# Kernel optimization log

Measured on AMD Instinct MI355X. Metric: run time of the kernel, lower is better.

The kernel has to match this reference:

```python
import jax, jax.numpy as jnp
import numpy as np

S, L, T, E, H = 512, 5, 20, 768, 64


def setup_inputs() -> dict:
    key = jax.random.key(0)
    ks = jax.random.split(key, 32)

    def p(k, shape, scale=0.05):
        return jax.random.normal(k, shape, dtype=jnp.float32) * scale

    return {
        "text_input": jax.random.normal(ks[0], (S, L, T, E), dtype=jnp.float32),
        "time_inputs": jax.random.uniform(ks[1], (S, L, T), dtype=jnp.float32),
        # TimeLSTM per-stock params (gate order f, i, o, c_tmp)
        "Wall": p(ks[2], (S, H, 4 * H)), "bWall": p(ks[3], (S, 4 * H)),
        "Uall": p(ks[4], (S, E, 4 * H)), "bUall": p(ks[5], (S, 4 * H)),
        "Wd": p(ks[6], (S, H, H)), "bWd": p(ks[7], (S, H)),
        # shared text/day Attention per stock
        "W1": p(ks[8], (S, H, H)), "b1": p(ks[9], (S, H)),
        "W2": p(ks[10], (S, H, H)), "b2": p(ks[11], (S, H)),
        "V": p(ks[12], (S, H, 1)), "bV": p(ks[13], (S, 1)),
        # day nn.LSTM per stock (gate order i, f, g, o)
        "Wih": p(ks[14], (S, H, 4 * H)), "Whh": p(ks[15], (S, H, 4 * H)),
        "bih": p(ks[16], (S, 4 * H)), "bhh": p(ks[17], (S, 4 * H)),
        # shared output head
        "lin_w": p(ks[18], (H, 1)), "lin_b": p(ks[19], (1,)),
        "no_stocks": S,
    }


def _forward(text_input, time_inputs, Wall, bWall, Uall, bUall, Wd, bWd,
             W1, b1, W2, b2, V, bV, Wih, Whh, bih, bhh, lin_w, lin_b, no_stocks):
    def per_stock(x, ts, Wall, bWall, Uall, bUall, Wd, bWd,
                  W1, b1, W2, b2, V, bV, Wih, Whh, bih, bhh):
        # x: [L, T, E], ts: [L, T] -- lookback days are an inner batch for the TimeLSTM
        u = jnp.einsum('lte,eg->ltg', x, Uall) + bUall  # [L, T, 4H]

        def step(carry, inp):
            h, c = carry                 # [L, H]
            u_t, ts_t = inp              # [L, 4H], [L]
            c_s1 = jnp.tanh(c @ Wd + bWd)
            c_adj = (c - c_s1) + c_s1 * ts_t[:, None]
            gates = h @ Wall + bWall + u_t
            f, i, o, c_tmp = jnp.split(gates, 4, axis=1)
            f = jax.nn.sigmoid(f)
            i = jax.nn.sigmoid(i)
            o = jax.nn.sigmoid(o)
            c_tmp = jax.nn.sigmoid(c_tmp)  # sigmoid (not tanh), faithful to source
            c_new = f * c_adj + i * c_tmp
            h_new = o * jnp.tanh(c_new)
            return (h_new, c_new), o     # module collects the o gate as 'outputs'

        init = (jnp.zeros((L, H), x.dtype), jnp.zeros((L, H), x.dtype))
        (h_fin, _), o_seq = jax.lax.scan(step, init, (u.transpose(1, 0, 2), ts.T))
        full = o_seq.transpose(1, 0, 2)  # [L, T, H]

        # text attention: score = V(tanh(W1(last) + W2(full))), softmax over T
        score = jnp.tanh((h_fin @ W1 + b1)[:, None, :] + full @ W2 + b2) @ V + bV  # [L, T, 1]
        aw = jax.nn.softmax(score, axis=1)
        text_vec = jnp.sum(aw * full, axis=1)  # [L, H]

        # day nn.LSTM: input (1, L, H) seq-first => one cell step with batch=L, zero state
        h0 = jnp.zeros((L, H), x.dtype)
        g = text_vec @ Wih + bih + h0 @ Whh + bhh
        gi, gf, gg, go = jnp.split(g, 4, axis=1)
        c_d = jax.nn.sigmoid(gi) * jnp.tanh(gg)  # f * c0 = 0
        h_d = jax.nn.sigmoid(go) * jnp.tanh(c_d)  # [L, H]; output == h_n here

        # day attention reuses the SAME text_attention weights; full == last == h_d
        s2 = jnp.tanh(h_d @ W1 + b1 + h_d @ W2 + b2) @ V + bV  # [L, 1]
        aw2 = jax.nn.softmax(s2, axis=0)
        return jnp.sum(aw2 * h_d, axis=0)  # [H]

    ft_vec = jax.vmap(per_stock)(text_input, time_inputs, Wall, bWall, Uall, bUall,
                                 Wd, bWd, W1, b1, W2, b2, V, bV,
                                 Wih, Whh, bih, bhh)  # [S, H]
    return jax.nn.leaky_relu(ft_vec @ lin_w + lin_b, negative_slope=0.01)  # [S, 1]


def reference(text_input, time_inputs, Wall, bWall, Uall, bUall, Wd, bWd,
              W1, b1, W2, b2, V, bV, Wih, Whh, bih, bhh, lin_w, lin_b, no_stocks):
    return _forward(text_input, time_inputs, Wall, bWall, Uall, bUall, Wd, bWd,
                    W1, b1, W2, b2, V, bV, Wih, Whh, bih, bhh, lin_w, lin_b, no_stocks)
```

## Files before the change

kernel.cpp:

```cpp
#include <hip/hip_runtime.h>
#include <cstddef>

#define NS 512
#define NL 5
#define NT 20
#define NE 768
#define NH 64
#define NG 256

__device__ __forceinline__ float sigf(float x) { return 1.0f / (1.0f + expf(-x)); }
__device__ __forceinline__ float bcast(float v, int k) {
    return __int_as_float(__builtin_amdgcn_readlane(__float_as_int(v), k));
}

typedef __attribute__((ext_vector_type(8))) short short8v;
typedef __attribute__((ext_vector_type(4))) float f32x4;

__device__ __forceinline__ void split_bf16(float x, unsigned short& hi, unsigned short& lo) {
    unsigned int bx = __float_as_uint(x);
    unsigned int h = (bx + 0x8000u) >> 16;
    hi = (unsigned short)h;
    float r = x - __uint_as_float(h << 16);
    lo = (unsigned short)((__float_as_uint(r) + 0x8000u) >> 16);
}

__global__ __launch_bounds__(512, 2) void k_gemm_u(
    const float* __restrict__ x, const float* __restrict__ U,
    const float* __restrict__ bU, float* __restrict__ u)
{
    __shared__ unsigned short Af[8 * 2 * 64 * 8];
    __shared__ unsigned short Bf[16 * 2 * 64 * 8];
    const int s = blockIdx.x;
    const int tid = threadIdx.x;
    const int wave = tid >> 6, lane = tid & 63;
    const int wm = wave & 1, wn = wave >> 1;
    const float* xg = x + (size_t)s * (NL * NT * NE);
    const float* Ug = U + (size_t)s * (NE * NG);

    f32x4 acc[4][4] = {};

    const int arow = tid >> 2, ab = tid & 3;
    const unsigned int a_off0 = (((unsigned)(arow >> 4) * 2 + 0) * 64 + ((arow & 15) + 16 * ab)) * 8;
    const unsigned int a_off1 = a_off0 + 64 * 8;
    const int bcol = tid & 255, bq1 = tid >> 8;
    const unsigned int b_base = (unsigned)(bcol >> 4) * 2 * 64 * 8;
    const unsigned int b_off1h = b_base + ((bcol & 15) + 16 * bq1) * 8;
    const unsigned int b_off1l = b_off1h + 64 * 8;
    const unsigned int b_off2h = b_base + ((bcol & 15) + 16 * (bq1 + 2)) * 8;
    const unsigned int b_off2l = b_off2h + 64 * 8;

    float av[8], bv1[8], bv2[8];
    {
        const float* pa = xg + (size_t)arow * NE + ab * 8;
        if (arow < 100) {
            float4 q0 = *(const float4*)pa, q1 = *(const float4*)(pa + 4);
            av[0]=q0.x; av[1]=q0.y; av[2]=q0.z; av[3]=q0.w;
            av[4]=q1.x; av[5]=q1.y; av[6]=q1.z; av[7]=q1.w;
        } else {
            #pragma unroll
            for (int j = 0; j < 8; ++j) av[j] = 0.0f;
        }
        const float* pb = Ug + bcol;
        #pragma unroll
        for (int j = 0; j < 8; ++j) {
            bv1[j] = pb[(size_t)(8 * bq1 + j) * NG];
            bv2[j] = pb[(size_t)(8 * bq1 + 16 + j) * NG];
        }
    }

    for (int st = 0; st < 24; ++st) {
        {
            unsigned short h[8], l[8];
            #pragma unroll
            for (int j = 0; j < 8; ++j) split_bf16(av[j], h[j], l[j]);
            uint4 ph, pl;
            ph.x = h[0] | (h[1] << 16); ph.y = h[2] | (h[3] << 16);
            ph.z = h[4] | (h[5] << 16); ph.w = h[6] | (h[7] << 16);
            pl.x = l[0] | (l[1] << 16); pl.y = l[2] | (l[3] << 16);
            pl.z = l[4] | (l[5] << 16); pl.w = l[6] | (l[7] << 16);
            *(uint4*)&Af[a_off0] = ph;
            *(uint4*)&Af[a_off1] = pl;
            #pragma unroll
            for (int j = 0; j < 8; ++j) split_bf16(bv1[j], h[j], l[j]);
            ph.x = h[0] | (h[1] << 16); ph.y = h[2] | (h[3] << 16);
            ph.z = h[4] | (h[5] << 16); ph.w = h[6] | (h[7] << 16);
            pl.x = l[0] | (l[1] << 16); pl.y = l[2] | (l[3] << 16);
            pl.z = l[4] | (l[5] << 16); pl.w = l[6] | (l[7] << 16);
            *(uint4*)&Bf[b_off1h] = ph;
            *(uint4*)&Bf[b_off1l] = pl;
            #pragma unroll
            for (int j = 0; j < 8; ++j) split_bf16(bv2[j], h[j], l[j]);
            ph.x = h[0] | (h[1] << 16); ph.y = h[2] | (h[3] << 16);
            ph.z = h[4] | (h[5] << 16); ph.w = h[6] | (h[7] << 16);
            pl.x = l[0] | (l[1] << 16); pl.y = l[2] | (l[3] << 16);
            pl.z = l[4] | (l[5] << 16); pl.w = l[6] | (l[7] << 16);
            *(uint4*)&Bf[b_off2h] = ph;
            *(uint4*)&Bf[b_off2l] = pl;
        }
        __syncthreads();

        if (st + 1 < 24) {
            const int k0 = (st + 1) * 32;
            const float* pa = xg + (size_t)arow * NE + k0 + ab * 8;
            if (arow < 100) {
                float4 q0 = *(const float4*)pa, q1 = *(const float4*)(pa + 4);
                av[0]=q0.x; av[1]=q0.y; av[2]=q0.z; av[3]=q0.w;
                av[4]=q1.x; av[5]=q1.y; av[6]=q1.z; av[7]=q1.w;
            } else {
                #pragma unroll
                for (int j = 0; j < 8; ++j) av[j] = 0.0f;
            }
            const float* pb = Ug + (size_t)k0 * NG + bcol;
            #pragma unroll
            for (int j = 0; j < 8; ++j) {
                bv1[j] = pb[(size_t)(8 * bq1 + j) * NG];
                bv2[j] = pb[(size_t)(8 * bq1 + 16 + j) * NG];
            }
        }

        short8v ah[4], al[4];
        #pragma unroll
        for (int mi = 0; mi < 4; ++mi) {
            const unsigned int mt = wm * 4 + mi;
            ah[mi] = *(const short8v*)&Af[(mt * 2 + 0) * 512 + lane * 8];
            al[mi] = *(const short8v*)&Af[(mt * 2 + 1) * 512 + lane * 8];
        }
        #pragma unroll
        for (int ni = 0; ni < 4; ++ni) {
            const unsigned int nt = wn * 4 + ni;
            short8v bh = *(const short8v*)&Bf[(nt * 2 + 0) * 512 + lane * 8];
            short8v bl = *(const short8v*)&Bf[(nt * 2 + 1) * 512 + lane * 8];
            #pragma unroll
            for (int mi = 0; mi < 4; ++mi) {
                acc[mi][ni] = __builtin_amdgcn_mfma_f32_16x16x32_bf16(ah[mi], bh, acc[mi][ni], 0, 0, 0);
                acc[mi][ni] = __builtin_amdgcn_mfma_f32_16x16x32_bf16(ah[mi], bl, acc[mi][ni], 0, 0, 0);
                acc[mi][ni] = __builtin_amdgcn_mfma_f32_16x16x32_bf16(al[mi], bh, acc[mi][ni], 0, 0, 0);
            }
        }
        __syncthreads();
    }

    const int c_sub = 4 * (lane >> 4);
    #pragma unroll
    for (int ni = 0; ni < 4; ++ni) {
        const int gcol = wn * 64 + ni * 16 + (lane & 15);
        const float bb = bU[(size_t)s * NG + gcol];
        #pragma unroll
        for (int mi = 0; mi < 4; ++mi) {
            const int grow0 = wm * 64 + mi * 16 + c_sub;
            #pragma unroll
            for (int r = 0; r < 4; ++r) {
                const int grow = grow0 + r;
                if (grow < 100) {
                    const int ld = grow / 20, td = grow % 20;
                    u[(((size_t)s * NT + td) * NL + ld) * NG + gcol] = acc[mi][ni][r] + bb;
                }
            }
        }
    }
}

#define WD    0
#define W1OFF 0
#define W2OFF 4096
#define FULLO 8192
#define HS    14592
#define TQ    14912
#define CA    15232
#define GATES 15552
#define TS    16832
#define SC    16932
#define B0    17032
#define B1    17096
#define BVV   17160
#define BV1   17224
#define SMTOT 17228

__global__ __launch_bounds__(320, 3) void k_stock(
    const float* __restrict__ u, const float* __restrict__ ti,
    const float* __restrict__ Wall, const float* __restrict__ bWall,
    const float* __restrict__ Wd, const float* __restrict__ bWd,
    const float* __restrict__ W1, const float* __restrict__ b1,
    const float* __restrict__ W2, const float* __restrict__ b2,
    const float* __restrict__ V, const float* __restrict__ bV,
    const float* __restrict__ Wih, const float* __restrict__ bih,
    const float* __restrict__ bhh, const float* __restrict__ lin_w,
    const float* __restrict__ lin_b, float* __restrict__ out)
{
    __shared__ float sm[SMTOT];
    const int s = blockIdx.x;
    const int tid = threadIdx.x;
    const int lq = tid >> 6, hh = tid & 63;
    const int lane = hh;
    const float* ug = u + (size_t)s * NT * NL * NG;

    for (int i = tid; i < 1024; i += 320)
        *(float4*)&sm[WD + i * 4] = *(const float4*)(Wd + (size_t)s * 4096 + i * 4);
    for (int i = tid; i < 1024; i += 320)
        *(float4*)&sm[W2OFF + i * 4] = *(const float4*)(W2 + (size_t)s * 4096 + i * 4);
    if (tid < NH) {
        sm[B0 + tid]  = b1[(size_t)s * NH + tid];
        sm[B1 + tid]  = b2[(size_t)s * NH + tid];
        sm[BVV + tid] = V[(size_t)s * NH + tid];
    }
    if (tid == 0) sm[BV1] = bV[s];
    if (tid < NL * NT) sm[TS + tid] = ti[(size_t)s * NL * NT + tid];
    sm[HS + tid] = 0.0f;
    const float bwd_r = bWd[(size_t)s * NH + hh];
    float c_reg = 0.0f;
    float wall_r[NH];
    float bwall_r = 0.0f, uc[NL];
    if (tid < NG) {
        bwall_r = bWall[(size_t)s * NG + tid];
        const float* wp = Wall + (size_t)s * (NH * NG) + tid;
        #pragma unroll
        for (int k = 0; k < NH; ++k) wall_r[k] = wp[(size_t)k * NG];
        #pragma unroll
        for (int l = 0; l < NL; ++l) uc[l] = ug[(size_t)l * NG + tid];
    }
    __syncthreads();

    for (int t = 0; t < NT; ++t) {
        float un[NL];
        if (tid < NG) {
            if (t + 1 < NT) {
                #pragma unroll
                for (int l = 0; l < NL; ++l)
                    un[l] = ug[(size_t)((t + 1) * NL + l) * NG + tid];
            } else {
                #pragma unroll
                for (int l = 0; l < NL; ++l) un[l] = 0.0f;
            }
            float hreg[NL];
            #pragma unroll
            for (int l = 0; l < NL; ++l) hreg[l] = sm[HS + l * NH + lane];
            float gv[NL];
            #pragma unroll
            for (int l = 0; l < NL; ++l) gv[l] = bwall_r + uc[l];
            #pragma unroll
            for (int k = 0; k < NH; ++k) {
                float w = wall_r[k];
                #pragma unroll
                for (int l = 0; l < NL; ++l)
                    gv[l] += bcast(hreg[l], k) * w;
            }
            #pragma unroll
            for (int l = 0; l < NL; ++l)
                sm[GATES + l * NG + tid] = sigf(gv[l]);
        }
        float ssum = bwd_r;
        #pragma unroll
        for (int k = 0; k < NH; ++k)
            ssum += bcast(c_reg, k) * sm[WD + k * NH + hh];
        float cs1 = tanhf(ssum);
        float ca = c_reg - cs1 + cs1 * sm[TS + lq * NT + t];
        __syncthreads();
        {
            float f  = sm[GATES + lq * NG + hh];
            float ii = sm[GATES + lq * NG + 64 + hh];
            float oo = sm[GATES + lq * NG + 128 + hh];
            float ct = sm[GATES + lq * NG + 192 + hh];
            float cn = f * ca + ii * ct;
            c_reg = cn;
            sm[HS + tid] = oo * tanhf(cn);
            sm[FULLO + (lq * NT + t) * NH + hh] = oo;
        }
        __syncthreads();
        if (tid < NG) {
            #pragma unroll
            for (int l = 0; l < NL; ++l) uc[l] = un[l];
        }
    }

    for (int i = tid; i < 1024; i += 320)
        *(float4*)&sm[W1OFF + i * 4] = *(const float4*)(W1 + (size_t)s * 4096 + i * 4);
    __syncthreads();

    {
        float qv = sm[B0 + hh];
        for (int k4 = 0; k4 < NH; k4 += 4) {
            float4 hv = *(const float4*)&sm[HS + lq * NH + k4];
            qv += hv.x * sm[W1OFF + (k4 + 0) * NH + hh]
                + hv.y * sm[W1OFF + (k4 + 1) * NH + hh]
                + hv.z * sm[W1OFF + (k4 + 2) * NH + hh]
                + hv.w * sm[W1OFF + (k4 + 3) * NH + hh];
        }
        sm[TQ + tid] = qv;
    }
    __syncthreads();

    for (int lt = lq; lt < NL * NT; lt += 5) {
        int l = lt / NT;
        float v = sm[TQ + l * NH + lane] + sm[B1 + lane];
        for (int k4 = 0; k4 < NH; k4 += 4) {
            float4 fv = *(const float4*)&sm[FULLO + lt * NH + k4];
            v += fv.x * sm[W2OFF + (k4 + 0) * NH + lane]
               + fv.y * sm[W2OFF + (k4 + 1) * NH + lane]
               + fv.z * sm[W2OFF + (k4 + 2) * NH + lane]
               + fv.w * sm[W2OFF + (k4 + 3) * NH + lane];
        }
        v = tanhf(v) * sm[BVV + lane];
        #pragma unroll
        for (int m = 32; m > 0; m >>= 1) v += __shfl_xor(v, m, 64);
        if (lane == 0) sm[SC + lt] = v + sm[BV1];
    }
    __syncthreads();

    if (tid < NL) {
        float mx = -1e30f;
        for (int t = 0; t < NT; ++t) mx = fmaxf(mx, sm[SC + tid * NT + t]);
        float sum = 0.0f;
        for (int t = 0; t < NT; ++t) {
            float e = expf(sm[SC + tid * NT + t] - mx);
            sm[SC + tid * NT + t] = e;
            sum += e;
        }
        float inv = 1.0f / sum;
        for (int t = 0; t < NT; ++t) sm[SC + tid * NT + t] *= inv;
    }
    __syncthreads();

    {
        float sv = 0.0f;
        #pragma unroll
        for (int t = 0; t < NT; ++t)
            sv += sm[SC + lq * NT + t] * sm[FULLO + (lq * NT + t) * NH + hh];
        sm[CA + tid] = sv;
    }
    __syncthreads();

    if (tid < NG) {
        float bsum = bih[(size_t)s * NG + tid] + bhh[(size_t)s * NG + tid];
        float d[NL];
        #pragma unroll
        for (int l = 0; l < NL; ++l) d[l] = bsum;
        for (int k = 0; k < NH; ++k) {
            float wk = Wih[((size_t)s * NH + k) * NG + tid];
            #pragma unroll
            for (int l = 0; l < NL; ++l)
                d[l] += sm[CA + l * NH + k] * wk;
        }
        #pragma unroll
        for (int l = 0; l < NL; ++l)
            sm[GATES + l * NG + tid] = d[l];
    }
    __syncthreads();
    {
        float gi = sm[GATES + lq * NG + hh];
        float gg = sm[GATES + lq * NG + 128 + hh];
        float go = sm[GATES + lq * NG + 192 + hh];
        float cd = sigf(gi) * tanhf(gg);
        sm[TQ + tid] = sigf(go) * tanhf(cd);
    }
    __syncthreads();

    {
        float v = sm[B0 + lane] + sm[B1 + lane];
        for (int k4 = 0; k4 < NH; k4 += 4) {
            float4 hv = *(const float4*)&sm[TQ + lq * NH + k4];
            v += hv.x * (sm[W1OFF + (k4 + 0) * NH + lane] + sm[W2OFF + (k4 + 0) * NH + lane])
               + hv.y * (sm[W1OFF + (k4 + 1) * NH + lane] + sm[W2OFF + (k4 + 1) * NH + lane])
               + hv.z * (sm[W1OFF + (k4 + 2) * NH + lane] + sm[W2OFF + (k4 + 2) * NH + lane])
               + hv.w * (sm[W1OFF + (k4 + 3) * NH + lane] + sm[W2OFF + (k4 + 3) * NH + lane]);
        }
        v = tanhf(v) * sm[BVV + lane];
        #pragma unroll
        for (int m = 32; m > 0; m >>= 1) v += __shfl_xor(v, m, 64);
        if (lane == 0) sm[SC + lq] = v + sm[BV1];
    }
    __syncthreads();
    if (tid == 0) {
        float mx = -1e30f;
        for (int l = 0; l < NL; ++l) mx = fmaxf(mx, sm[SC + l]);
        float sum = 0.0f;
        for (int l = 0; l < NL; ++l) {
            float e = expf(sm[SC + l] - mx);
            sm[SC + l] = e;
            sum += e;
        }
        float inv = 1.0f / sum;
        for (int l = 0; l < NL; ++l) sm[SC + l] *= inv;
    }
    __syncthreads();

    if (tid < NH) {
        float fv = 0.0f;
        #pragma unroll
        for (int l = 0; l < NL; ++l)
            fv += sm[SC + l] * sm[TQ + l * NH + tid];
        fv *= lin_w[tid];
        #pragma unroll
        for (int m = 32; m > 0; m >>= 1) fv += __shfl_xor(fv, m, 64);
        if (tid == 0) {
            float val = fv + lin_b[0];
            out[s] = val > 0.0f ? val : 0.01f * val;
        }
    }
}

extern "C" void kernel_launch(void* const* d_in, const int* in_sizes, int n_in,
                              void* d_out, int out_size, void* d_ws, size_t ws_size,
                              hipStream_t stream) {
    (void)in_sizes; (void)n_in; (void)out_size; (void)ws_size;
    const float* x     = (const float*)d_in[0];
    const float* ti    = (const float*)d_in[1];
    const float* Wall  = (const float*)d_in[2];
    const float* bWall = (const float*)d_in[3];
    const float* Uall  = (const float*)d_in[4];
    const float* bUall = (const float*)d_in[5];
    const float* Wd    = (const float*)d_in[6];
    const float* bWd   = (const float*)d_in[7];
    const float* W1    = (const float*)d_in[8];
    const float* b1    = (const float*)d_in[9];
    const float* W2    = (const float*)d_in[10];
    const float* b2    = (const float*)d_in[11];
    const float* V     = (const float*)d_in[12];
    const float* bV    = (const float*)d_in[13];
    const float* Wih   = (const float*)d_in[14];
    const float* bih   = (const float*)d_in[16];
    const float* bhh   = (const float*)d_in[17];
    const float* lin_w = (const float*)d_in[18];
    const float* lin_b = (const float*)d_in[19];
    float* out = (float*)d_out;
    float* u = (float*)d_ws;

    k_gemm_u<<<NS, 512, 0, stream>>>(x, Uall, bUall, u);
    k_stock<<<NS, 320, 0, stream>>>(u, ti, Wall, bWall, Wd, bWd, W1, b1, W2, b2,
                                    V, bV, Wih, bih, bhh, lin_w, lin_b, out);
}
```

Baseline: 942.0 us.

## Split stock kernel into recurrence and post-attention kernels via workspace

Splits the monolithic per-stock kernel into a recurrence kernel with a much smaller shared-memory footprint and a separate post-processing kernel. The output-gate history and final hidden state are written into the already-consumed u workspace instead of shared memory, then reloaded by the second kernel. The aim is to raise occupancy of the recurrence kernel by shrinking LDS use and tightening launch bounds. The cost is an extra kernel launch, a global-memory round trip for the intermediates, and possible register pressure from the tighter launch bound.

```diff
diff --git a/kernel.cpp b/kernel.cpp
--- a/kernel.cpp
+++ b/kernel.cpp
@@ -160,52 +160,28 @@
     }
 }
 
-#define WD    0
-#define W1OFF 0
-#define W2OFF 4096
-#define FULLO 8192
-#define HS    14592
-#define TQ    14912
-#define CA    15232
-#define GATES 15552
-#define TS    16832
-#define SC    16932
-#define B0    17032
-#define B1    17096
-#define BVV   17160
-#define BV1   17224
-#define SMTOT 17228
-
-__global__ __launch_bounds__(320, 3) void k_stock(
-    const float* __restrict__ u, const float* __restrict__ ti,
+#define R_WD    0
+#define R_GATES 4096
+#define R_HS    5376
+#define R_TS    5696
+#define R_TOT   5796
+
+__global__ __launch_bounds__(320, 4) void k_recur(
+    float* __restrict__ u, const float* __restrict__ ti,
     const float* __restrict__ Wall, const float* __restrict__ bWall,
-    const float* __restrict__ Wd, const float* __restrict__ bWd,
-    const float* __restrict__ W1, const float* __restrict__ b1,
-    const float* __restrict__ W2, const float* __restrict__ b2,
-    const float* __restrict__ V, const float* __restrict__ bV,
-    const float* __restrict__ Wih, const float* __restrict__ bih,
-    const float* __restrict__ bhh, const float* __restrict__ lin_w,
-    const float* __restrict__ lin_b, float* __restrict__ out)
+    const float* __restrict__ Wd, const float* __restrict__ bWd)
 {
-    __shared__ float sm[SMTOT];
+    __shared__ float sm[R_TOT];
     const int s = blockIdx.x;
     const int tid = threadIdx.x;
     const int lq = tid >> 6, hh = tid & 63;
     const int lane = hh;
-    const float* ug = u + (size_t)s * NT * NL * NG;
+    float* ug = u + (size_t)s * NT * NL * NG;
 
     for (int i = tid; i < 1024; i += 320)
-        *(float4*)&sm[WD + i * 4] = *(const float4*)(Wd + (size_t)s * 4096 + i * 4);
-    for (int i = tid; i < 1024; i += 320)
-        *(float4*)&sm[W2OFF + i * 4] = *(const float4*)(W2 + (size_t)s * 4096 + i * 4);
-    if (tid < NH) {
-        sm[B0 + tid]  = b1[(size_t)s * NH + tid];
-        sm[B1 + tid]  = b2[(size_t)s * NH + tid];
-        sm[BVV + tid] = V[(size_t)s * NH + tid];
-    }
-    if (tid == 0) sm[BV1] = bV[s];
-    if (tid < NL * NT) sm[TS + tid] = ti[(size_t)s * NL * NT + tid];
-    sm[HS + tid] = 0.0f;
+        *(float4*)&sm[R_WD + i * 4] = *(const float4*)(Wd + (size_t)s * 4096 + i * 4);
+    if (tid < NL * NT) sm[R_TS + tid] = ti[(size_t)s * NL * NT + tid];
+    sm[R_HS + tid] = 0.0f;
     const float bwd_r = bWd[(size_t)s * NH + hh];
     float c_reg = 0.0f;
     float wall_r[NH];
@@ -233,7 +209,7 @@
             }
             float hreg[NL];
             #pragma unroll
-            for (int l = 0; l < NL; ++l) hreg[l] = sm[HS + l * NH + lane];
+            for (int l = 0; l < NL; ++l) hreg[l] = sm[R_HS + l * NH + lane];
             float gv[NL];
             #pragma unroll
             for (int l = 0; l < NL; ++l) gv[l] = bwall_r + uc[l];
@@ -246,24 +222,24 @@
             }
             #pragma unroll
             for (int l = 0; l < NL; ++l)
-                sm[GATES + l * NG + tid] = sigf(gv[l]);
+                sm[R_GATES + l * NG + tid] = sigf(gv[l]);
         }
         float ssum = bwd_r;
         #pragma unroll
         for (int k = 0; k < NH; ++k)
-            ssum += bcast(c_reg, k) * sm[WD + k * NH + hh];
+            ssum += bcast(c_reg, k) * sm[R_WD + k * NH + hh];
         float cs1 = tanhf(ssum);
-        float ca = c_reg - cs1 + cs1 * sm[TS + lq * NT + t];
+        float ca = c_reg - cs1 + cs1 * sm[R_TS + lq * NT + t];
         __syncthreads();
         {
-            float f  = sm[GATES + lq * NG + hh];
-            float ii = sm[GATES + lq * NG + 64 + hh];
-            float oo = sm[GATES + lq * NG + 128 + hh];
-            float ct = sm[GATES + lq * NG + 192 + hh];
+            float f  = sm[R_GATES + lq * NG + hh];
+            float ii = sm[R_GATES + lq * NG + 64 + hh];
+            float oo = sm[R_GATES + lq * NG + 128 + hh];
+            float ct = sm[R_GATES + lq * NG + 192 + hh];
             float cn = f * ca + ii * ct;
             c_reg = cn;
-            sm[HS + tid] = oo * tanhf(cn);
-            sm[FULLO + (lq * NT + t) * NH + hh] = oo;
+            sm[R_HS + tid] = oo * tanhf(cn);
+            ug[(size_t)(t * NL + lq) * NG + hh] = oo;
         }
         __syncthreads();
         if (tid < NG) {
@@ -271,52 +247,99 @@
             for (int l = 0; l < NL; ++l) uc[l] = un[l];
         }
     }
+    ug[(size_t)(0 * NL + lq) * NG + 64 + hh] = sm[R_HS + tid];
+}
+
+#define P_W1    0
+#define P_W2    4096
+#define P_FULLO 8192
+#define P_HS    14592
+#define P_TQ    14912
+#define P_CA    15232
+#define P_SC    15552
+#define P_B0    15652
+#define P_B1    15716
+#define P_BVV   15780
+#define P_BV1   15844
+#define P_TOT   15848
+
+__global__ __launch_bounds__(320, 2) void k_post(
+    const float* __restrict__ u,
+    const float* __restrict__ W1, const float* __restrict__ b1,
+    const float* __restrict__ W2, const float* __restrict__ b2,
+    const float* __restrict__ V, const float* __restrict__ bV,
+    const float* __restrict__ Wih, const float* __restrict__ bih,
+    const float* __restrict__ bhh, const float* __restrict__ lin_w,
+    const float* __restrict__ lin_b, float* __restrict__ out)
+{
+    __shared__ float sm[P_TOT];
+    const int s = blockIdx.x;
+    const int tid = threadIdx.x;
+    const int lq = tid >> 6, hh = tid & 63;
+    const int lane = hh;
+    const float* ug = u + (size_t)s * NT * NL * NG;
 
     for (int i = tid; i < 1024; i += 320)
-        *(float4*)&sm[W1OFF + i * 4] = *(const float4*)(W1 + (size_t)s * 4096 + i * 4);
+        *(float4*)&sm[P_W1 + i * 4] = *(const float4*)(W1 + (size_t)s * 4096 + i * 4);
+    for (int i = tid; i < 1024; i += 320)
+        *(float4*)&sm[P_W2 + i * 4] = *(const float4*)(W2 + (size_t)s * 4096 + i * 4);
+    for (int i = tid; i < 1600; i += 320) {
+        const int idx = i >> 4;
+        const int l = idx / NT, t = idx % NT;
+        const int k4 = (i & 15) * 4;
+        *(float4*)&sm[P_FULLO + idx * NH + k4] =
+            *(const float4*)(ug + (size_t)(t * NL + l) * NG + k4);
+    }
+    sm[P_HS + tid] = ug[(size_t)(0 * NL + lq) * NG + 64 + hh];
+    if (tid < NH) {
+        sm[P_B0 + tid]  = b1[(size_t)s * NH + tid];
+        sm[P_B1 + tid]  = b2[(size_t)s * NH + tid];
+        sm[P_BVV + tid] = V[(size_t)s * NH + tid];
+    }
+    if (tid == 0) sm[P_BV1] = bV[s];
     __syncthreads();
 
     {
-        float qv = sm[B0 + hh];
+        float qv = sm[P_B0 + hh];
         for (int k4 = 0; k4 < NH; k4 += 4) {
-            float4 hv = *(const float4*)&sm[HS + lq * NH + k4];
-            qv += hv.x * sm[W1OFF + (k4 + 0) * NH + hh]
-                + hv.y * sm[W1OFF + (k4 + 1) * NH + hh]
-                + hv.z * sm[W1OFF + (k4 + 2) * NH + hh]
-                + hv.w * sm[W1OFF + (k4 + 3) * NH + hh];
-        }
-        sm[TQ + tid] = qv;
+            float4 hv = *(const float4*)&sm[P_HS + lq * NH + k4];
+            qv += hv.x * sm[P_W1 + (k4 + 0) * NH + hh]
+                + hv.y * sm[P_W1 + (k4 + 1) * NH + hh]
+                + hv.z * sm[P_W1 + (k4 + 2) * NH + hh]
+                + hv.w * sm[P_W1 + (k4 + 3) * NH + hh];
+        }
+        sm[P_TQ + tid] = qv;
     }
     __syncthreads();
 
     for (int lt = lq; lt < NL * NT; lt += 5) {
         int l = lt / NT;
-        float v = sm[TQ + l * NH + lane] + sm[B1 + lane];
+        float v = sm[P_TQ + l * NH + lane] + sm[P_B1 + lane];
         for (int k4 = 0; k4 < NH; k4 += 4) {
-            float4 fv = *(const float4*)&sm[FULLO + lt * NH + k4];
-            v += fv.x * sm[W2OFF + (k4 + 0) * NH + lane]
-               + fv.y * sm[W2OFF + (k4 + 1) * NH + lane]
-               + fv.z * sm[W2OFF + (k4 + 2) * NH + lane]
-               + fv.w * sm[W2OFF + (k4 + 3) * NH + lane];
-        }
-        v = tanhf(v) * sm[BVV + lane];
+            float4 fv = *(const float4*)&sm[P_FULLO + lt * NH + k4];
+            v += fv.x * sm[P_W2 + (k4 + 0) * NH + lane]
+               + fv.y * sm[P_W2 + (k4 + 1) * NH + lane]
+               + fv.z * sm[P_W2 + (k4 + 2) * NH + lane]
+               + fv.w * sm[P_W2 + (k4 + 3) * NH + lane];
+        }
+        v = tanhf(v) * sm[P_BVV + lane];
         #pragma unroll
         for (int m = 32; m > 0; m >>= 1) v += __shfl_xor(v, m, 64);
-        if (lane == 0) sm[SC + lt] = v + sm[BV1];
+        if (lane == 0) sm[P_SC + lt] = v + sm[P_BV1];
     }
     __syncthreads();
 
     if (tid < NL) {
         float mx = -1e30f;
-        for (int t = 0; t < NT; ++t) mx = fmaxf(mx, sm[SC + tid * NT + t]);
+        for (int t = 0; t < NT; ++t) mx = fmaxf(mx, sm[P_SC + tid * NT + t]);
         float sum = 0.0f;
         for (int t = 0; t < NT; ++t) {
-            float e = expf(sm[SC + tid * NT + t] - mx);
-            sm[SC + tid * NT + t] = e;
+            float e = expf(sm[P_SC + tid * NT + t] - mx);
+            sm[P_SC + tid * NT + t] = e;
             sum += e;
         }
         float inv = 1.0f / sum;
-        for (int t = 0; t < NT; ++t) sm[SC + tid * NT + t] *= inv;
+        for (int t = 0; t < NT; ++t) sm[P_SC + tid * NT + t] *= inv;
     }
     __syncthreads();
 
@@ -324,8 +347,8 @@
         float sv = 0.0f;
         #pragma unroll
         for (int t = 0; t < NT; ++t)
-            sv += sm[SC + lq * NT + t] * sm[FULLO + (lq * NT + t) * NH + hh];
-        sm[CA + tid] = sv;
+            sv += sm[P_SC + lq * NT + t] * sm[P_FULLO + (lq * NT + t) * NH + hh];
+        sm[P_CA + tid] = sv;
     }
     __syncthreads();
 
@@ -338,48 +361,48 @@
             float wk = Wih[((size_t)s * NH + k) * NG + tid];
             #pragma unroll
             for (int l = 0; l < NL; ++l)
-                d[l] += sm[CA + l * NH + k] * wk;
+                d[l] += sm[P_CA + l * NH + k] * wk;
         }
         #pragma unroll
         for (int l = 0; l < NL; ++l)
-            sm[GATES + l * NG + tid] = d[l];
+            sm[P_FULLO + l * NG + tid] = d[l];
     }
     __syncthreads();
     {
-        float gi = sm[GATES + lq * NG + hh];
-        float gg = sm[GATES + lq * NG + 128 + hh];
-        float go = sm[GATES + lq * NG + 192 + hh];
+        float gi = sm[P_FULLO + lq * NG + hh];
+        float gg = sm[P_FULLO + lq * NG + 128 + hh];
+        float go = sm[P_FULLO + lq * NG + 192 + hh];
         float cd = sigf(gi) * tanhf(gg);
-        sm[TQ + tid] = sigf(go) * tanhf(cd);
+        sm[P_TQ + tid] = sigf(go) * tanhf(cd);
     }
     __syncthreads();
 
     {
-        float v = sm[B0 + lane] + sm[B1 + lane];
+        float v = sm[P_B0 + lane] + sm[P_B1 + lane];
         for (int k4 = 0; k4 < NH; k4 += 4) {
-            float4 hv = *(const float4*)&sm[TQ + lq * NH + k4];
-            v += hv.x * (sm[W1OFF + (k4 + 0) * NH + lane] + sm[W2OFF + (k4 + 0) * NH + lane])
-               + hv.y * (sm[W1OFF + (k4 + 1) * NH + lane] + sm[W2OFF + (k4 + 1) * NH + lane])
-               + hv.z * (sm[W1OFF + (k4 + 2) * NH + lane] + sm[W2OFF + (k4 + 2) * NH + lane])
-               + hv.w * (sm[W1OFF + (k4 + 3) * NH + lane] + sm[W2OFF + (k4 + 3) * NH + lane]);
-        }
-        v = tanhf(v) * sm[BVV + lane];
+            float4 hv = *(const float4*)&sm[P_TQ + lq * NH + k4];
+            v += hv.x * (sm[P_W1 + (k4 + 0) * NH + lane] + sm[P_W2 + (k4 + 0) * NH + lane])
+               + hv.y * (sm[P_W1 + (k4 + 1) * NH + lane] + sm[P_W2 + (k4 + 1) * NH + lane])
+               + hv.z * (sm[P_W1 + (k4 + 2) * NH + lane] + sm[P_W2 + (k4 + 2) * NH + lane])
+               + hv.w * (sm[P_W1 + (k4 + 3) * NH + lane] + sm[P_W2 + (k4 + 3) * NH + lane]);
+        }
+        v = tanhf(v) * sm[P_BVV + lane];
         #pragma unroll
         for (int m = 32; m > 0; m >>= 1) v += __shfl_xor(v, m, 64);
-        if (lane == 0) sm[SC + lq] = v + sm[BV1];
+        if (lane == 0) sm[P_SC + lq] = v + sm[P_BV1];
     }
     __syncthreads();
     if (tid == 0) {
         float mx = -1e30f;
-        for (int l = 0; l < NL; ++l) mx = fmaxf(mx, sm[SC + l]);
+        for (int l = 0; l < NL; ++l) mx = fmaxf(mx, sm[P_SC + l]);
         float sum = 0.0f;
         for (int l = 0; l < NL; ++l) {
-            float e = expf(sm[SC + l] - mx);
-            sm[SC + l] = e;
+            float e = expf(sm[P_SC + l] - mx);
+            sm[P_SC + l] = e;
             sum += e;
         }
         float inv = 1.0f / sum;
-        for (int l = 0; l < NL; ++l) sm[SC + l] *= inv;
+        for (int l = 0; l < NL; ++l) sm[P_SC + l] *= inv;
     }
     __syncthreads();
 
@@ -387,7 +410,7 @@
         float fv = 0.0f;
         #pragma unroll
         for (int l = 0; l < NL; ++l)
-            fv += sm[SC + l] * sm[TQ + l * NH + tid];
+            fv += sm[P_SC + l] * sm[P_TQ + l * NH + tid];
         fv *= lin_w[tid];
         #pragma unroll
         for (int m = 32; m > 0; m >>= 1) fv += __shfl_xor(fv, m, 64);
@@ -425,6 +448,7 @@
     float* u = (float*)d_ws;
 
     k_gemm_u<<<NS, 512, 0, stream>>>(x, Uall, bUall, u);
-    k_stock<<<NS, 320, 0, stream>>>(u, ti, Wall, bWall, Wd, bWd, W1, b1, W2, b2,
-                                    V, bV, Wih, bih, bhh, lin_w, lin_b, out);
-}
+    k_recur<<<NS, 320, 0, stream>>>(u, ti, Wall, bWall, Wd, bWd);
+    k_post<<<NS, 320, 0, stream>>>(u, W1, b1, W2, b2, V, bV,
+                                   Wih, bih, bhh, lin_w, lin_b, out);
+}
```

New measurement: 879.5 us. 1.07x faster.
